# Performance work log

Hardware: AMD Instinct MI355X
Metric: run time of the kernel (lower is better)

The kernel has to match this reference:

```python
import jax, jax.numpy as jnp
import numpy as np

M1, M2, M3 = 12, 12, 8
WIDTH = 32


def _spectral_conv(v, wr, wi):
    # v: [B, C, X, Y, T]; wr/wi: [4, Ci, Co, M1, M2, M3]
    B, C, X, Y, T = v.shape
    vft = jnp.fft.rfftn(v, axes=(-3, -2, -1))  # [B,C,X,Y,T//2+1] complex
    w = wr.astype(jnp.complex64) + 1j * wi.astype(jnp.complex64)
    mul = lambda blk, ww: jnp.einsum('bixyz,ioxyz->boxyz', blk, ww)
    out = jnp.zeros((B, wr.shape[2], X, Y, T // 2 + 1), dtype=vft.dtype)
    out = out.at[:, :, :M1, :M2, :M3].set(mul(vft[:, :, :M1, :M2, :M3], w[0]))
    out = out.at[:, :, -M1:, :M2, :M3].set(mul(vft[:, :, -M1:, :M2, :M3], w[1]))
    out = out.at[:, :, :M1, -M2:, :M3].set(mul(vft[:, :, :M1, -M2:, :M3], w[2]))
    out = out.at[:, :, -M1:, -M2:, :M3].set(mul(vft[:, :, -M1:, -M2:, :M3], w[3]))
    return jnp.fft.irfftn(out, s=(X, Y, T), axes=(-3, -2, -1))


def _conv1x1(v, w, b):
    # v: [B,C,X,Y,T]; w: [Co,Ci]; b: [Co]
    return jnp.einsum('bixyz,oi->boxyz', v, w) + b[None, :, None, None, None]


def setup_inputs() -> dict:
    key = jax.random.key(0)
    ks = jax.random.split(key, 24)
    B, X, Y, T = 8, 64, 64, 40
    W = WIDTH
    scale = 1.0 / (W * W)
    d = {}
    d['h'] = jax.random.normal(ks[0], (B, X, Y, T, 2), dtype=jnp.float32)
    d['x'] = jax.random.normal(ks[1], (B, X, Y, T, 3), dtype=jnp.float32)
    d['fc0_w'] = jax.random.normal(ks[2], (5, W), dtype=jnp.float32) * 0.3
    d['fc0_b'] = jnp.zeros((W,), dtype=jnp.float32)
    for i, name in enumerate(['sc0', 'sc1', 'sc3']):
        d[name + '_wr'] = scale * jax.random.uniform(ks[3 + 2 * i], (4, W, W, M1, M2, M3), dtype=jnp.float32)
        d[name + '_wi'] = scale * jax.random.uniform(ks[4 + 2 * i], (4, W, W, M1, M2, M3), dtype=jnp.float32)
    for i, name in enumerate(['w0', 'w1', 'w3']):
        d[name + '_w'] = jax.random.normal(ks[9 + 2 * i], (W, W), dtype=jnp.float32) * (1.0 / np.sqrt(W))
        d[name + '_b'] = jnp.zeros((W,), dtype=jnp.float32)
    d['fc1_w'] = jax.random.normal(ks[15], (W, 64), dtype=jnp.float32) * (1.0 / np.sqrt(W))
    d['fc1_b'] = jnp.zeros((64,), dtype=jnp.float32)
    d['fc2_w'] = jax.random.normal(ks[16], (64, 2), dtype=jnp.float32) * 0.125
    d['fc2_b'] = jnp.zeros((2,), dtype=jnp.float32)
    return d


def reference(h, x, fc0_w, fc0_b, sc0_wr, sc0_wi, sc1_wr, sc1_wi, sc3_wr, sc3_wi,
              w0_w, w0_b, w1_w, w1_b, w3_w, w3_b, fc1_w, fc1_b, fc2_w, fc2_b):
    v = jnp.concatenate((h, x), axis=-1)                 # [B,X,Y,T,5]
    v = v @ fc0_w + fc0_b                                # lift to width
    v = jnp.transpose(v, (0, 4, 1, 2, 3))                # [B,W,X,Y,T]
    v = jax.nn.gelu(_spectral_conv(v, sc0_wr, sc0_wi) + _conv1x1(v, w0_w, w0_b), approximate=False)
    v = jax.nn.gelu(_spectral_conv(v, sc1_wr, sc1_wi) + _conv1x1(v, w1_w, w1_b), approximate=False)
    v = _spectral_conv(v, sc3_wr, sc3_wi) + _conv1x1(v, w3_w, w3_b)
    v = jnp.transpose(v, (0, 2, 3, 4, 1))                # [B,X,Y,T,W]
    v = jax.nn.gelu(v @ fc1_w + fc1_b, approximate=False)
    return v @ fc2_w + fc2_b                             # [B,X,Y,T,2]
```

## Files before the change

kernel.cpp:

```cpp
#include <hip/hip_runtime.h>
#include <math.h>

#define BATCH 8
#define WID   32
#define NX    64
#define NY    64
#define NT    40
#define M1C   12
#define KT    8
#define KXC   24
#define KYC   24
#define NXY   (NX*NY)
#define NXYT  (NXY*NT)
#define NP    (BATCH*NXYT)

#define TWO_PI 6.283185307179586f

static __device__ __forceinline__ float gelu_f(float v){
  return 0.5f*v*(1.0f + erff(v*0.7071067811865476f));
}

static __device__ __forceinline__ void barrier_lds(){
  asm volatile("s_waitcnt lgkmcnt(0)\n\ts_barrier" ::: "memory");
}


__global__ __launch_bounds__(256) void k_fc0(const float* __restrict__ h, const float* __restrict__ x,
                                             const float* __restrict__ w, const float* __restrict__ b,
                                             float* __restrict__ V){
  __shared__ float sw[160], sb[32];
  int tid=threadIdx.x;
  if(tid<160) sw[tid]=w[tid];
  if(tid<32)  sb[tid]=b[tid];
  __syncthreads();
  int pl = tid>>3, q = tid&7;
  int p = blockIdx.x*32 + pl;
  float i0=h[(size_t)p*2], i1=h[(size_t)p*2+1];
  float i2=x[(size_t)p*3], i3=x[(size_t)p*3+1], i4=x[(size_t)p*3+2];
  int c0=q*4;
  float4 o;
  float* po=(float*)&o;
  #pragma unroll
  for(int u=0;u<4;u++){
    int c=c0+u;
    po[u] = sb[c] + i0*sw[c] + i1*sw[32+c] + i2*sw[64+c] + i3*sw[96+c] + i4*sw[128+c];
  }
  ((float4*)V)[(size_t)p*8 + q] = o;
}

__global__ __launch_bounds__(256) void k_fwd_ty(const float* __restrict__ V, float2* __restrict__ F2){
  __shared__ __align__(16) unsigned char smem[61696];
  float*  vt    = (float*)smem;
  float2* f2out = (float2*)smem;
  float2* twy   = (float2*)(smem + 49408);
  int tid = threadIdx.x;
  int b = blockIdx.x >> 6, x = blockIdx.x & 63;
  int c = tid & 31, k = tid >> 5;
  for(int i=tid;i<KYC*NY;i+=256){
    int ky=i/NY, y=i-ky*NY;
    int f = ky<M1C ? ky : ky+40;
    float ang = -TWO_PI*(float)((f*y)%NY)/(float)NY;
    twy[ky*NY+y] = make_float2(cosf(ang), sinf(ang));
  }
  float2 twr[NT];
  #pragma unroll
  for(int t=0;t<NT;t++){
    float ang = -TWO_PI*(float)((k*t)%NT)/(float)NT;
    twr[t] = make_float2(cosf(ang), sinf(ang));
  }
  float2 acc[KYC];
  #pragma unroll
  for(int ky=0;ky<KYC;ky++) acc[ky]=make_float2(0.f,0.f);
  const float4* src = (const float4*)(V + (size_t)(b*NX+x)*(NY*NT*WID));
  for(int g=0; g<8; g++){
    __syncthreads();
    #pragma unroll
    for(int r=0;r<10;r++) ((float4*)vt)[r*256+tid] = src[g*2560 + r*256 + tid];
    __syncthreads();
    for(int yl=0; yl<8; yl+=2){
      float sr0=0.f, si0=0.f, sr1=0.f, si1=0.f;
      const float* vp0 = vt + yl*1280 + c;
      const float* vp1 = vp0 + 1280;
      #pragma unroll
      for(int t=0;t<NT;t++){
        float2 w = twr[t];
        float v0 = vp0[t*32];
        float v1 = vp1[t*32];
        sr0 += v0*w.x; si0 += v0*w.y;
        sr1 += v1*w.x; si1 += v1*w.y;
      }
      int y = g*8 + yl;
      #pragma unroll
      for(int ky=0;ky<KYC;ky++){
        float4 wy = *(const float4*)&twy[ky*NY + y];
        acc[ky].x += sr0*wy.x - si0*wy.y + sr1*wy.z - si1*wy.w;
        acc[ky].y += sr0*wy.y + si0*wy.x + sr1*wy.w + si1*wy.z;
      }
    }
  }
  __syncthreads();
  #pragma unroll
  for(int ky=0;ky<KYC;ky++) f2out[c*193 + ky*KT + k] = acc[ky];
  __syncthreads();
  for(int i=tid;i<WID*KYC*KT;i+=256){
    int cc=i/192, e=i-cc*192;
    F2[((size_t)(b*WID+cc)*NX + x)*(KYC*KT) + e] = f2out[cc*193 + e];
  }
}

__global__ __launch_bounds__(256) void k_fwd_x(const float2* __restrict__ F2, float2* __restrict__ F3){
  __shared__ float2 tile[NX*KT];
  __shared__ float2 twi[KXC*65];
  int tid=threadIdx.x;
  int bc = blockIdx.x / KYC;
  int ky = blockIdx.x - bc*KYC;
  for(int i=tid;i<NX*KT;i+=256){
    int xx=i/KT, kt=i-xx*KT;
    tile[i] = F2[((size_t)bc*NX + xx)*(KYC*KT) + ky*KT + kt];
  }
  for(int i=tid;i<KXC*NX;i+=256){
    int kx=i/NX, xx=i-kx*NX;
    int f = kx<M1C ? kx : kx+40;
    float ang = -TWO_PI*(float)((f*xx)%NX)/(float)NX;
    twi[kx*65+xx] = make_float2(cosf(ang), sinf(ang));
  }
  __syncthreads();
  for(int item=tid; item<KXC*KT; item+=256){
    int kx=item/KT, kt=item-kx*KT;
    float sr=0.f, si=0.f;
    #pragma unroll 8
    for(int xx=0;xx<NX;xx++){
      float2 a = tile[xx*KT+kt];
      float2 w = twi[kx*65+xx];
      sr += a.x*w.x - a.y*w.y;
      si += a.x*w.y + a.y*w.x;
    }
    F3[(size_t)bc*(KXC*KYC*KT) + kx*(KYC*KT) + ky*KT + kt] = make_float2(sr,si);
  }
}

__global__ __launch_bounds__(256) void k_mix(const float2* __restrict__ F3, const float* __restrict__ wr,
                                             const float* __restrict__ wi, float2* __restrict__ F4){
  __shared__ float2 f3s[BATCH*WID*KT];
  int tid = threadIdx.x;
  int kx = blockIdx.x / KYC, ky = blockIdx.x - kx*KYC;
  int mode0 = blockIdx.x * KT;
  int xp = (kx>=M1C), yp = (ky>=M1C);
  int m1 = kx - M1C*xp, m2 = ky - M1C*yp;
  int blk = xp + 2*yp;
  for(int i=tid;i<1024;i+=256){
    int row=i>>2, q=i&3;
    ((float4*)f3s)[row*4+q] = ((const float4*)(F3 + (size_t)row*4608 + mode0))[q];
  }
  int o = tid>>3, kt = tid&7;
  size_t wbase = (size_t)blk*1179648 + (size_t)o*1152 + m1*96 + m2*8 + kt;
  float wre[WID], wim[WID];
  #pragma unroll
  for(int i=0;i<WID;i++){
    wre[i] = wr[wbase + (size_t)i*36864];
    wim[i] = wi[wbase + (size_t)i*36864];
  }
  __syncthreads();
  #pragma unroll
  for(int b=0;b<BATCH;b++){
    float ar=0.f, ai=0.f;
    #pragma unroll
    for(int i=0;i<WID;i++){
      float2 a = f3s[(b*WID+i)*KT + kt];
      ar += a.x*wre[i] - a.y*wim[i];
      ai += a.x*wim[i] + a.y*wre[i];
    }
    F4[(size_t)(b*WID+o)*4608 + mode0 + kt] = make_float2(ar,ai);
  }
}

__global__ __launch_bounds__(256) void k_inv_x(const float2* __restrict__ F4, float2* __restrict__ F2){
  __shared__ float2 tile[KXC*KT];
  __shared__ float2 twi[NX*25];
  int tid=threadIdx.x;
  int bc = blockIdx.x / KYC, ky = blockIdx.x - (blockIdx.x/KYC)*KYC;
  for(int i=tid;i<KXC*KT;i+=256){
    int kx=i/KT, kt=i-kx*KT;
    tile[i] = F4[(size_t)bc*4608 + kx*(KYC*KT) + ky*KT + kt];
  }
  for(int i=tid;i<NX*KXC;i+=256){
    int xx=i/KXC, kx=i-xx*KXC;
    int f = kx<M1C ? kx : kx+40;
    float ang = TWO_PI*(float)((f*xx)%NX)/(float)NX;
    twi[xx*25+kx] = make_float2(cosf(ang)*(1.0f/64.0f), sinf(ang)*(1.0f/64.0f));
  }
  __syncthreads();
  for(int item=tid; item<NX*KT; item+=256){
    int xx=item/KT, kt=item-xx*KT;
    float sr=0.f, si=0.f;
    #pragma unroll 8
    for(int kx=0;kx<KXC;kx++){
      float2 a = tile[kx*KT+kt];
      float2 w = twi[xx*25+kx];
      sr += a.x*w.x - a.y*w.y;
      si += a.x*w.y + a.y*w.x;
    }
    F2[((size_t)bc*NX + xx)*(KYC*KT) + ky*KT + kt] = make_float2(sr,si);
  }
}

template<bool GELU>
__global__ __launch_bounds__(256) void k_conv(const float2* __restrict__ F2, const float* __restrict__ wcv,
                                              const float* __restrict__ bcv, float* __restrict__ V){
  __shared__ __align__(16) unsigned char smem[24576];
  float*  vt0  = (float*)smem;
  float*  vt1  = (float*)(smem+5120);
  float2* ftc  = (float2*)(smem+10240);
  float2* tcts = (float2*)(smem+12288);
  float2* twy  = (float2*)(smem+14848);
  float2* f2h  = (float2*)smem;

  int tid=threadIdx.x;
  int b  = blockIdx.x >> 7;
  int x  = (blockIdx.x >> 1) & 63;
  int y0 = (blockIdx.x & 1) * 32;
  int cid = tid & 31, ktid = tid >> 5;
  int oid = tid & 31, tg  = tid >> 5;

  float2 fr[KYC];
  #pragma unroll
  for(int half=0; half<2; half++){
    for(int i=tid;i<1536;i+=256){
      int cc=i/96, q=i-cc*96;
      ((float4*)f2h)[i] = *((const float4*)(F2 + ((size_t)(b*WID + half*16 + cc)*NX + x)*(KYC*KT)) + q);
    }
    __syncthreads();
    if((cid>>4) == half){
      const float2* fp = f2h + (cid&15)*192 + ktid;
      #pragma unroll
      for(int ky=0;ky<KYC;ky++) fr[ky] = fp[ky*8];
    }
    __syncthreads();
  }
  float wreg[WID];
  #pragma unroll
  for(int cc=0;cc<WID;cc++) wreg[cc] = wcv[oid*WID + cc];
  float breg = bcv[oid];
  for(int i=tid;i<KT*NT;i+=256){
    int k=i/NT, t=i-k*NT;
    float ang = TWO_PI*(float)((k*t)%NT)/(float)NT;
    float sc = (k==0 ? 1.0f : 2.0f)*(1.0f/(float)NT);
    tcts[i] = make_float2(cosf(ang)*sc, sinf(ang)*sc);
  }
  for(int i=tid;i<32*KYC;i+=256){
    int yy=i/KYC, ky=i-yy*KYC;
    int f = ky<M1C ? ky : ky+40;
    float ang = TWO_PI*(float)((f*(y0+yy))%NY)/(float)NY;
    twy[i] = make_float2(cosf(ang)*(1.0f/64.0f), sinf(ang)*(1.0f/64.0f));
  }
  float* plane = V + (size_t)((b*NX+x)*NY + y0)*(NT*WID);
  const float4* gp = (const float4*)plane;
  bool has2 = tid < 64;
  float4 g0 = gp[tid];
  float4 g1 = has2 ? gp[256+tid] : make_float4(0,0,0,0);
  ((float4*)vt0)[tid] = g0;
  if(has2) ((float4*)vt0)[256+tid] = g1;
  __syncthreads();

  for(int y=0;y<32;y++){
    if(y+1 < 32){
      g0 = gp[(size_t)(y+1)*320 + tid];
      if(has2) g1 = gp[(size_t)(y+1)*320 + 256 + tid];
    }
    {
      const float2* tw = twy + y*KYC;
      float sr=0.f, si=0.f;
      #pragma unroll
      for(int ky=0;ky<KYC;ky++){
        float2 w = tw[ky];
        float2 a = fr[ky];
        sr += a.x*w.x - a.y*w.y;
        si += a.x*w.y + a.y*w.x;
      }
      ftc[ktid*32 + cid] = make_float2(sr,si);
    }
    barrier_lds();
    {
      float2 fR[KT];
      #pragma unroll
      for(int k=0;k<KT;k++) fR[k] = ftc[k*32 + oid];
      const float* vb = (y&1) ? vt1 : vt0;
      float* outp = plane + (size_t)y*(NT*WID);
      #pragma unroll
      for(int j=0;j<5;j++){
        int t = tg*5 + j;
        float a = breg;
        const float* vrow = vb + t*32;
        #pragma unroll
        for(int c4=0;c4<WID;c4+=4){
          float4 vv = *(const float4*)(vrow + c4);
          a += vv.x*wreg[c4] + vv.y*wreg[c4+1] + vv.z*wreg[c4+2] + vv.w*wreg[c4+3];
        }
        #pragma unroll
        for(int k=0;k<KT;k++){
          float2 w = tcts[k*NT + t];
          a += fR[k].x*w.x - fR[k].y*w.y;
        }
        outp[t*32 + oid] = GELU ? gelu_f(a) : a;
      }
    }
    if(y+1 < 32){
      float* d = (y&1) ? vt0 : vt1;
      ((float4*)d)[tid] = g0;
      if(has2) ((float4*)d)[256+tid] = g1;
    }
    barrier_lds();
  }
}

__global__ __launch_bounds__(256) void k_mlp(const float* __restrict__ V, const float* __restrict__ w1,
                                             const float* __restrict__ b1, const float* __restrict__ w2,
                                             const float* __restrict__ b2, float* __restrict__ out){
  __shared__ float sw1t[64*WID];
  __shared__ float sb1[64], sw2[128], sb2[2];
  int tid=threadIdx.x;
  for(int i=tid;i<64*WID;i+=256){ int j=i>>5, c=i&31; sw1t[i]=w1[c*64+j]; }
  if(tid<64) sb1[tid]=b1[tid];
  if(tid<128) sw2[tid]=w2[tid];
  if(tid<2) sb2[tid]=b2[tid];
  __syncthreads();
  size_t p0 = (size_t)blockIdx.x*1024 + (size_t)tid*4;
  float vv[128];
  const float4* vp = (const float4*)(V + p0*WID);
  #pragma unroll
  for(int q=0;q<32;q++) *((float4*)(vv+4*q)) = vp[q];
  float oa[8];
  #pragma unroll
  for(int pt=0;pt<4;pt++){ oa[2*pt]=sb2[0]; oa[2*pt+1]=sb2[1]; }
  #pragma unroll 4
  for(int j=0;j<64;j++){
    float a0=sb1[j], a1=a0, a2=a0, a3=a0;
    const float* wrow = sw1t + j*WID;
    #pragma unroll
    for(int c4=0;c4<WID;c4+=4){
      float4 w = *(const float4*)(wrow + c4);
      a0 += vv[     c4]*w.x + vv[     c4+1]*w.y + vv[     c4+2]*w.z + vv[     c4+3]*w.w;
      a1 += vv[32 + c4]*w.x + vv[32 + c4+1]*w.y + vv[32 + c4+2]*w.z + vv[32 + c4+3]*w.w;
      a2 += vv[64 + c4]*w.x + vv[64 + c4+1]*w.y + vv[64 + c4+2]*w.z + vv[64 + c4+3]*w.w;
      a3 += vv[96 + c4]*w.x + vv[96 + c4+1]*w.y + vv[96 + c4+2]*w.z + vv[96 + c4+3]*w.w;
    }
    a0=gelu_f(a0); a1=gelu_f(a1); a2=gelu_f(a2); a3=gelu_f(a3);
    float u0=sw2[2*j], u1=sw2[2*j+1];
    oa[0]+=a0*u0; oa[1]+=a0*u1; oa[2]+=a1*u0; oa[3]+=a1*u1;
    oa[4]+=a2*u0; oa[5]+=a2*u1; oa[6]+=a3*u0; oa[7]+=a3*u1;
  }
  float4* op = (float4*)(out + p0*2);
  op[0]=make_float4(oa[0],oa[1],oa[2],oa[3]);
  op[1]=make_float4(oa[4],oa[5],oa[6],oa[7]);
}

extern "C" void kernel_launch(void* const* d_in, const int* in_sizes, int n_in,
                              void* d_out, int out_size, void* d_ws, size_t ws_size,
                              hipStream_t stream){
  const float* h     = (const float*)d_in[0];
  const float* x     = (const float*)d_in[1];
  const float* fc0_w = (const float*)d_in[2];
  const float* fc0_b = (const float*)d_in[3];
  const float* scwr[3] = {(const float*)d_in[4], (const float*)d_in[6], (const float*)d_in[8]};
  const float* scwi[3] = {(const float*)d_in[5], (const float*)d_in[7], (const float*)d_in[9]};
  const float* cw[3]   = {(const float*)d_in[10], (const float*)d_in[12], (const float*)d_in[14]};
  const float* cb[3]   = {(const float*)d_in[11], (const float*)d_in[13], (const float*)d_in[15]};
  const float* fc1_w = (const float*)d_in[16];
  const float* fc1_b = (const float*)d_in[17];
  const float* fc2_w = (const float*)d_in[18];
  const float* fc2_b = (const float*)d_in[19];

  const size_t VSZ = (size_t)BATCH*WID*NXYT;
  float*  V  = (float*)d_ws;
  float2* F2 = (float2*)(V + VSZ);
  float2* F4 = F2 + (size_t)BATCH*WID*NX*KYC*KT;
  float2* F3 = (float2*)d_out;

  k_fc0<<<NP/32, 256, 0, stream>>>(h, x, fc0_w, fc0_b, V);
  for(int L=0; L<3; L++){
    k_fwd_ty<<<BATCH*NX, 256, 0, stream>>>(V, F2);
    k_fwd_x<<<(BATCH*WID)*KYC, 256, 0, stream>>>(F2, F3);
    k_mix<<<KXC*KYC, 256, 0, stream>>>(F3, scwr[L], scwi[L], F4);
    k_inv_x<<<(BATCH*WID)*KYC, 256, 0, stream>>>(F4, F2);
    if(L<2) k_conv<true ><<<BATCH*NX*2, 256, 0, stream>>>(F2, cw[L], cb[L], V);
    else    k_conv<false><<<BATCH*NX*2, 256, 0, stream>>>(F2, cw[L], cb[L], V);
  }
  k_mlp<<<NP/1024, 256, 0, stream>>>(V, fc1_w, fc1_b, fc2_w, fc2_b, (float*)d_out);
}
```

Before: 1.585 ms.

## Factor inverse T-DFT twiddles into per-group rotation and constant tables, double-buffer ftc

The inverse real DFT over time in k_conv is restructured. Each thread group's time block offset becomes a per-thread twiddle rotation held in registers, and the inner 5-point twiddles become compile-time constant tables. This removes the shared-memory cos/sin table and its per-output LDS reads. The k scaling is folded into the y-frequency coefficients once. The ftc staging buffer is double-buffered so the second barrier per y iteration can be dropped, at the cost of more registers and careful buffer-reuse correctness.

```diff
diff --git a/kernel.cpp b/kernel.cpp
--- a/kernel.cpp
+++ b/kernel.cpp
@@ -210,9 +210,9 @@
   __shared__ __align__(16) unsigned char smem[24576];
   float*  vt0  = (float*)smem;
   float*  vt1  = (float*)(smem+5120);
-  float2* ftc  = (float2*)(smem+10240);
-  float2* tcts = (float2*)(smem+12288);
-  float2* twy  = (float2*)(smem+14848);
+  float2* ftc0 = (float2*)(smem+10240);
+  float2* ftc1 = (float2*)(smem+12288);
+  float2* twy  = (float2*)(smem+14336);
   float2* f2h  = (float2*)smem;
 
   int tid=threadIdx.x;
@@ -237,15 +237,20 @@
     }
     __syncthreads();
   }
+  {
+    float ts = (ktid==0 ? 1.0f : 2.0f) * (1.0f/(float)NT);
+    #pragma unroll
+    for(int ky=0;ky<KYC;ky++){ fr[ky].x *= ts; fr[ky].y *= ts; }
+  }
   float wreg[WID];
   #pragma unroll
   for(int cc=0;cc<WID;cc++) wreg[cc] = wcv[oid*WID + cc];
   float breg = bcv[oid];
-  for(int i=tid;i<KT*NT;i+=256){
-    int k=i/NT, t=i-k*NT;
-    float ang = TWO_PI*(float)((k*t)%NT)/(float)NT;
-    float sc = (k==0 ? 1.0f : 2.0f)*(1.0f/(float)NT);
-    tcts[i] = make_float2(cosf(ang)*sc, sinf(ang)*sc);
+  float2 twtg[KT];
+  #pragma unroll
+  for(int k=0;k<KT;k++){
+    float ang = 0.78539816339744831f*(float)((k*tg)&7);
+    twtg[k] = make_float2(cosf(ang), sinf(ang));
   }
   for(int i=tid;i<32*KYC;i+=256){
     int yy=i/KYC, ky=i-yy*KYC;
@@ -262,11 +267,33 @@
   if(has2) ((float4*)vt0)[256+tid] = g1;
   __syncthreads();
 
+  constexpr float CJ[KT][5] = {
+    {1.f, 1.f,          1.f,          1.f,          1.f         },
+    {1.f, 0.98768834f,  0.95105652f,  0.89100652f,  0.80901699f },
+    {1.f, 0.95105652f,  0.80901699f,  0.58778525f,  0.30901699f },
+    {1.f, 0.89100652f,  0.58778525f,  0.15643447f, -0.30901699f },
+    {1.f, 0.80901699f,  0.30901699f, -0.30901699f, -0.80901699f },
+    {1.f, 0.70710678f,  0.f,         -0.70710678f, -1.f         },
+    {1.f, 0.58778525f, -0.30901699f, -0.95105652f, -0.80901699f },
+    {1.f, 0.45399050f, -0.58778525f, -0.98768834f, -0.30901699f },
+  };
+  constexpr float SJ[KT][5] = {
+    {0.f, 0.f,          0.f,          0.f,          0.f         },
+    {0.f, 0.15643447f,  0.30901699f,  0.45399050f,  0.58778525f },
+    {0.f, 0.30901699f,  0.58778525f,  0.80901699f,  0.95105652f },
+    {0.f, 0.45399050f,  0.80901699f,  0.98768834f,  0.95105652f },
+    {0.f, 0.58778525f,  0.95105652f,  0.95105652f,  0.58778525f },
+    {0.f, 0.70710678f,  1.f,          0.70710678f,  0.f         },
+    {0.f, 0.80901699f,  0.95105652f,  0.30901699f, -0.58778525f },
+    {0.f, 0.89100652f,  0.80901699f, -0.15643447f, -0.95105652f },
+  };
+
   for(int y=0;y<32;y++){
     if(y+1 < 32){
       g0 = gp[(size_t)(y+1)*320 + tid];
       if(has2) g1 = gp[(size_t)(y+1)*320 + 256 + tid];
     }
+    float2* ftcb = (y&1) ? ftc1 : ftc0;
     {
       const float2* tw = twy + y*KYC;
       float sr=0.f, si=0.f;
@@ -277,30 +304,33 @@
         sr += a.x*w.x - a.y*w.y;
         si += a.x*w.y + a.y*w.x;
       }
-      ftc[ktid*32 + cid] = make_float2(sr,si);
+      ftcb[ktid*32 + cid] = make_float2(sr,si);
     }
     barrier_lds();
     {
-      float2 fR[KT];
-      #pragma unroll
-      for(int k=0;k<KT;k++) fR[k] = ftc[k*32 + oid];
+      float acc[5];
+      #pragma unroll
+      for(int j=0;j<5;j++) acc[j] = breg;
+      #pragma unroll
+      for(int k=0;k<KT;k++){
+        float2 f = ftcb[k*32 + oid];
+        float gx = f.x*twtg[k].x - f.y*twtg[k].y;
+        float gy = f.x*twtg[k].y + f.y*twtg[k].x;
+        #pragma unroll
+        for(int j=0;j<5;j++) acc[j] += gx*CJ[k][j] - gy*SJ[k][j];
+      }
       const float* vb = (y&1) ? vt1 : vt0;
       float* outp = plane + (size_t)y*(NT*WID);
       #pragma unroll
       for(int j=0;j<5;j++){
         int t = tg*5 + j;
-        float a = breg;
+        float a = acc[j];
         const float* vrow = vb + t*32;
         #pragma unroll
         for(int c4=0;c4<WID;c4+=4){
           float4 vv = *(const float4*)(vrow + c4);
           a += vv.x*wreg[c4] + vv.y*wreg[c4+1] + vv.z*wreg[c4+2] + vv.w*wreg[c4+3];
         }
-        #pragma unroll
-        for(int k=0;k<KT;k++){
-          float2 w = tcts[k*NT + t];
-          a += fR[k].x*w.x - fR[k].y*w.y;
-        }
         outp[t*32 + oid] = GELU ? gelu_f(a) : a;
       }
     }
@@ -309,7 +339,6 @@
       ((float4*)d)[tid] = g0;
       if(has2) ((float4*)d)[256+tid] = g1;
     }
-    barrier_lds();
   }
 }
 
```

Result: no change. 1.555 ms (-1.9%).
